# Optimization experiments

Measured on AMD Instinct MI355X. Metric: run time of the kernel, lower is better.

The kernel has to match this reference:

```python
import jax, jax.numpy as jnp
import numpy as np
import math


def setup_inputs() -> dict:
    key = jax.random.key(0)
    kq, kk, kv = jax.random.split(key, 3)
    B, H, S, D = 8, 12, 4096, 64
    q = jax.random.normal(kq, (B, H, S, D), dtype=jnp.float32)
    k = jax.random.normal(kk, (B, H, S, D), dtype=jnp.float32)
    v = jax.random.normal(kv, (B, H, S, D), dtype=jnp.float32)
    return {"q": q, "k": k, "v": v}


def reference(q, k, v):
    B, H, S, D = q.shape
    topk = int(2 * math.sqrt(S))  # 128 for S=4096
    # importance = mean + std (torch.std is unbiased -> ddof=1)
    importance = q.mean(axis=-1) + jnp.std(q, axis=-1, ddof=1)  # [B,H,S]
    _, idx = jax.lax.top_k(importance, topk)  # [B,H,topk]
    idx_e = idx[..., None]  # [B,H,topk,1]
    q_s = jnp.take_along_axis(q, idx_e, axis=2)  # [B,H,topk,D]
    k_s = jnp.take_along_axis(k, idx_e, axis=2)
    v_s = jnp.take_along_axis(v, idx_e, axis=2)
    scores = jnp.einsum('bhtd,bhsd->bhts', q_s, k_s) / math.sqrt(D)
    attn = jax.nn.softmax(scores, axis=-1)
    out_s = jnp.einsum('bhts,bhsd->bhtd', attn, v_s)  # [B,H,topk,D]
    # scatter back into a full tensor (torch uses empty_like; we use zeros
    # for the unselected positions so the output is deterministic)
    bI = jnp.arange(B)[:, None, None]
    hI = jnp.arange(H)[None, :, None]
    out = jnp.zeros_like(v).at[bI, hI, idx].set(out_s)  # [B,H,S,D]
    Himg = int(math.sqrt(S))
    return out.reshape(B, -1, Himg, Himg)  # [B, H*D, Himg, Himg]
```

## Files before the change

### kernel.cpp

```cpp
#include <hip/hip_runtime.h>
#include <hip/hip_fp16.h>
#include <math.h>

#define BH_N 96
#define S_N 4096
#define D_N 64
#define TOPK 128

typedef unsigned long long ull;

__device__ __forceinline__ ull orderKey(double d) {
  ull u = (ull)__double_as_longlong(d);
  if (u & 0x8000000000000000ULL) u = ~u;
  else u |= 0x8000000000000000ULL;
  return u;
}

__global__ __launch_bounds__(256)
void imp_zero_kernel(const float* __restrict__ q, float* __restrict__ out,
                     ull* __restrict__ keys) {
  const int tid = threadIdx.x;
  const size_t off = (size_t)blockIdx.x * 1024 + (size_t)tid * 4;
  const float4 v = *reinterpret_cast<const float4*>(q + off);
  float4 z; z.x = z.y = z.z = z.w = 0.f;
  *reinterpret_cast<float4*>(out + off) = z;

  double s  = (double)v.x + (double)v.y + (double)v.z + (double)v.w;
  double ss = (double)v.x * v.x + (double)v.y * v.y +
              (double)v.z * v.z + (double)v.w * v.w;
#pragma unroll
  for (int m = 1; m < 16; m <<= 1) {
    s  += __shfl_xor(s, m, 64);
    ss += __shfl_xor(ss, m, 64);
  }
  if ((tid & 15) == 0) {
    double mean = s * (1.0 / 64.0);
    double var = (ss - s * s * (1.0 / 64.0)) * (1.0 / 63.0);
    if (var < 0.0) var = 0.0;
    keys[(size_t)blockIdx.x * 16 + (tid >> 4)] = orderKey(mean + sqrt(var));
  }
}

__global__ __launch_bounds__(1024)
void sel_kernel(const ull* __restrict__ keys, int* __restrict__ idx_out) {
  __shared__ int red[2][16];
  __shared__ int s_idx[TOPK];
  __shared__ int s_tidx[1024];
  __shared__ int s_cnt, s_tcnt;

  const int tid = threadIdx.x;
  const int lane = tid & 63;
  const int wv = tid >> 6;
  const int bh = blockIdx.x;
  const ull* kb = keys + (size_t)bh * S_N;

  ull key[4];
#pragma unroll
  for (int i = 0; i < 4; ++i) key[i] = kb[i * 1024 + tid];

  if (tid == 0) { s_cnt = 0; s_tcnt = 0; }

  ull lo = 0ULL, hi = ~0ULL;
  int p = 0;
  while (lo < hi) {
    ull d = hi - lo;
    ull mid = lo + (d >> 1) + (d & 1ULL);
    int c = 0;
#pragma unroll
    for (int i = 0; i < 4; ++i) c += __popcll(__ballot(key[i] >= mid));
    if (lane == 0) red[p][wv] = c;
    __syncthreads();
    int total = 0;
#pragma unroll
    for (int w = 0; w < 16; ++w) total += red[p][w];
    if (total >= TOPK) lo = mid; else hi = mid - 1;
    p ^= 1;
  }
  const ull T = lo;

#pragma unroll
  for (int i = 0; i < 4; ++i) {
    if (key[i] > T) {
      int slot = atomicAdd(&s_cnt, 1);
      s_idx[slot] = i * 1024 + tid;
    } else if (key[i] == T) {
      int sl = atomicAdd(&s_tcnt, 1);
      if (sl < 1024) s_tidx[sl] = i * 1024 + tid;
    }
  }
  __syncthreads();
  const int nsel = s_cnt;
  const int need = TOPK - nsel;
  if (wv == 0 && need > 0) {
    int t = s_tcnt < 1024 ? s_tcnt : 1024;
    for (int sel = 0; sel < need; ++sel) {
      int mymin = 0x7fffffff;
      for (int j = lane; j < t; j += 64) mymin = min(mymin, s_tidx[j]);
#pragma unroll
      for (int m = 1; m < 64; m <<= 1) mymin = min(mymin, __shfl_xor(mymin, m, 64));
      if (lane == 0) s_idx[nsel + sel] = mymin;
      for (int j = lane; j < t; j += 64)
        if (s_tidx[j] == mymin) s_tidx[j] = 0x7fffffff;
    }
  }
  __syncthreads();
  if (tid < TOPK) idx_out[bh * TOPK + tid] = s_idx[tid];
}

__global__ __launch_bounds__(256)
void attn_kernel(const float* __restrict__ q, const float* __restrict__ k,
                 const float* __restrict__ v, const int* __restrict__ idx_all,
                 float* __restrict__ out) {
  __shared__ __align__(16) float sQ[32 * 65];
  __shared__ __align__(16) float sB[64 * 65];
  __shared__ __align__(16) __half sP[32 * 132];
  __shared__ int s_idx[TOPK];

  const int tid = threadIdx.x;
  const int bh = blockIdx.x >> 2;
  const int sub = blockIdx.x & 3;
  if (tid < TOPK) s_idx[tid] = idx_all[bh * TOPK + tid];

  const size_t base = (size_t)bh * S_N * D_N;
  const int rgrp = tid >> 4;
  const int c4 = (tid & 15) * 4;
  const int rr = tid >> 4;
  const int cc = tid & 15;

  __syncthreads();

#pragma unroll
  for (int it = 0; it < 2; ++it) {
    int r = it * 16 + rgrp;
    int srow = s_idx[sub * 32 + r];
    float4 val = *reinterpret_cast<const float4*>(q + base + (size_t)srow * D_N + c4);
    sQ[r * 65 + c4 + 0] = val.x; sQ[r * 65 + c4 + 1] = val.y;
    sQ[r * 65 + c4 + 2] = val.z; sQ[r * 65 + c4 + 3] = val.w;
  }

  float acc[2][8];
#pragma unroll
  for (int j = 0; j < 2; ++j)
#pragma unroll
    for (int m = 0; m < 8; ++m) acc[j][m] = 0.f;

  for (int h = 0; h < 2; ++h) {
    __syncthreads();
#pragma unroll
    for (int it = 0; it < 4; ++it) {
      int r = it * 16 + rgrp;
      int srow = s_idx[h * 64 + r];
      float4 val = *reinterpret_cast<const float4*>(k + base + (size_t)srow * D_N + c4);
      sB[r * 65 + c4 + 0] = val.x; sB[r * 65 + c4 + 1] = val.y;
      sB[r * 65 + c4 + 2] = val.z; sB[r * 65 + c4 + 3] = val.w;
    }
    __syncthreads();
    for (int kk = 0; kk < 64; kk += 2) {
#pragma unroll
      for (int u = 0; u < 2; ++u) {
        float qv0 = sQ[(2 * rr + 0) * 65 + kk + u];
        float qv1 = sQ[(2 * rr + 1) * 65 + kk + u];
        float kv[4];
#pragma unroll
        for (int m = 0; m < 4; ++m) kv[m] = sB[(cc * 4 + m) * 65 + kk + u];
#pragma unroll
        for (int m = 0; m < 4; ++m) {
          acc[0][h * 4 + m] += qv0 * kv[m];
          acc[1][h * 4 + m] += qv1 * kv[m];
        }
      }
    }
  }

  float rmax[2], rsum[2];
#pragma unroll
  for (int j = 0; j < 2; ++j) {
    float mx = acc[j][0];
#pragma unroll
    for (int m = 1; m < 8; ++m) mx = fmaxf(mx, acc[j][m]);
    rmax[j] = mx;
  }
#pragma unroll
  for (int mm = 1; mm < 16; mm <<= 1)
#pragma unroll
    for (int j = 0; j < 2; ++j) rmax[j] = fmaxf(rmax[j], __shfl_xor(rmax[j], mm, 64));
#pragma unroll
  for (int j = 0; j < 2; ++j) {
    float sum = 0.f;
#pragma unroll
    for (int m = 0; m < 8; ++m) {
      float pe = __expf(0.125f * (acc[j][m] - rmax[j]));
      acc[j][m] = pe;
      sum += pe;
    }
    rsum[j] = sum;
  }
#pragma unroll
  for (int mm = 1; mm < 16; mm <<= 1)
#pragma unroll
    for (int j = 0; j < 2; ++j) rsum[j] += __shfl_xor(rsum[j], mm, 64);
#pragma unroll
  for (int j = 0; j < 2; ++j) {
    float rinv = 1.f / rsum[j];
#pragma unroll
    for (int h2 = 0; h2 < 2; ++h2)
#pragma unroll
      for (int m = 0; m < 4; ++m) {
        int col = h2 * 64 + cc * 4 + m;
        sP[(2 * rr + j) * 132 + col] = __float2half_rn(acc[j][h2 * 4 + m] * rinv);
      }
  }

  float acc2[2][4];
#pragma unroll
  for (int j = 0; j < 2; ++j)
#pragma unroll
    for (int m = 0; m < 4; ++m) acc2[j][m] = 0.f;

  for (int h = 0; h < 2; ++h) {
    __syncthreads();
#pragma unroll
    for (int it = 0; it < 4; ++it) {
      int r = it * 16 + rgrp;
      int srow = s_idx[h * 64 + r];
      float4 val = *reinterpret_cast<const float4*>(v + base + (size_t)srow * D_N + c4);
      sB[r * 65 + c4 + 0] = val.x; sB[r * 65 + c4 + 1] = val.y;
      sB[r * 65 + c4 + 2] = val.z; sB[r * 65 + c4 + 3] = val.w;
    }
    __syncthreads();
    for (int s2 = 0; s2 < 64; ++s2) {
      int scol = h * 64 + s2;
      float pj0 = __half2float(sP[(2 * rr + 0) * 132 + scol]);
      float pj1 = __half2float(sP[(2 * rr + 1) * 132 + scol]);
      float vm[4];
#pragma unroll
      for (int m = 0; m < 4; ++m) vm[m] = sB[s2 * 65 + cc * 4 + m];
#pragma unroll
      for (int m = 0; m < 4; ++m) {
        acc2[0][m] += pj0 * vm[m];
        acc2[1][m] += pj1 * vm[m];
      }
    }
  }

#pragma unroll
  for (int j = 0; j < 2; ++j) {
    int srow = s_idx[sub * 32 + 2 * rr + j];
    float4 val;
    val.x = acc2[j][0]; val.y = acc2[j][1]; val.z = acc2[j][2]; val.w = acc2[j][3];
    *reinterpret_cast<float4*>(out + base + (size_t)srow * D_N + cc * 4) = val;
  }
}

extern "C" void kernel_launch(void* const* d_in, const int* in_sizes, int n_in,
                              void* d_out, int out_size, void* d_ws, size_t ws_size,
                              hipStream_t stream) {
  const float* q = (const float*)d_in[0];
  const float* k = (const float*)d_in[1];
  const float* v = (const float*)d_in[2];
  float* out = (float*)d_out;
  ull* keys = (ull*)d_ws;
  int* idx = (int*)((char*)d_ws + (size_t)BH_N * S_N * 8);

  imp_zero_kernel<<<24576, 256, 0, stream>>>(q, out, keys);
  sel_kernel<<<BH_N, 1024, 0, stream>>>(keys, idx);
  attn_kernel<<<BH_N * 4, 256, 0, stream>>>(q, k, v, idx, out);
}
```

Measured before the change: 308.2 us.

## Fuse importance, top-k selection and attention into one cooperative kernel

Merges the three kernels into one cooperative launch of 384 blocks. Each block computes importance keys and zeroes the output for its slice, then waits at a grid-wide sync, then redoes the top-k threshold search for its (b,h) inside a 256-thread block and runs the attention directly. Tie handling moves from a serial min-extraction loop to ballot-based prefix ranking, so the index buffer in global memory is no longer needed. In exchange the selection work is repeated four times per head and the code depends on cooperative-launch support, with a two-kernel fallback if that launch fails.

```diff
diff --git a/kernel.cpp b/kernel.cpp
--- a/kernel.cpp
+++ b/kernel.cpp
@@ -1,19 +1,299 @@
 #include <hip/hip_runtime.h>
 #include <hip/hip_fp16.h>
+#include <hip/hip_cooperative_groups.h>
 #include <math.h>
 
 #define BH_N 96
 #define S_N 4096
 #define D_N 64
 #define TOPK 128
+#define NBLK 384
+#define UNITS_TOTAL 24576
 
 typedef unsigned long long ull;
+namespace cg = cooperative_groups;
 
 __device__ __forceinline__ ull orderKey(double d) {
   ull u = (ull)__double_as_longlong(d);
   if (u & 0x8000000000000000ULL) u = ~u;
   else u |= 0x8000000000000000ULL;
   return u;
+}
+
+struct SharedMem {
+  int red[2][4];
+  int redG[4], redT[4], redS[4];
+  int s_idx[TOPK];
+  __align__(16) float sB[64 * 65];
+  __align__(16) unsigned char uQP[32 * 132 * 2];
+};
+
+__device__ __forceinline__ void sel_attn_body(
+    const float* __restrict__ q, const float* __restrict__ k,
+    const float* __restrict__ v, const ull* __restrict__ keys,
+    float* __restrict__ out, SharedMem& sm, int bh, int sub) {
+  const int tid = threadIdx.x;
+  const int lane = tid & 63;
+  const int wv = tid >> 6;
+
+  ull key[16];
+  {
+    const ull* kb = keys + (size_t)bh * S_N;
+#pragma unroll
+    for (int j = 0; j < 16; ++j) key[j] = kb[tid * 16 + j];
+  }
+
+  ull lo = 0ULL, hi = ~0ULL;
+  int p = 0;
+  while (lo < hi) {
+    ull d = hi - lo;
+    ull mid = lo + (d >> 1) + (d & 1ULL);
+    int c = 0;
+#pragma unroll
+    for (int j = 0; j < 16; ++j) c += __popcll(__ballot(key[j] >= mid));
+    if (lane == 0) sm.red[p][wv] = c;
+    __syncthreads();
+    int total = sm.red[p][0] + sm.red[p][1] + sm.red[p][2] + sm.red[p][3];
+    if (total >= TOPK) lo = mid; else hi = mid - 1;
+    p ^= 1;
+  }
+  const ull T = lo;
+
+  {
+    int cgt = 0, ctie = 0;
+#pragma unroll
+    for (int j = 0; j < 16; ++j) {
+      cgt  += __popcll(__ballot(key[j] > T));
+      ctie += __popcll(__ballot(key[j] == T));
+    }
+    if (lane == 0) { sm.redG[wv] = cgt; sm.redT[wv] = ctie; }
+  }
+  __syncthreads();
+  const int need = TOPK - (sm.redG[0] + sm.redG[1] + sm.redG[2] + sm.redG[3]);
+  int wTieBase = 0;
+#pragma unroll
+  for (int w = 0; w < 4; ++w) if (w < wv) wTieBase += sm.redT[w];
+
+  const ull below = (1ULL << lane) - 1ULL;
+  unsigned selBits = 0;
+  {
+    int lanesBelowTies = 0;
+#pragma unroll
+    for (int j = 0; j < 16; ++j)
+      lanesBelowTies += __popcll(__ballot(key[j] == T) & below);
+    int sameLane = 0;
+#pragma unroll
+    for (int j = 0; j < 16; ++j) {
+      const bool isTie = (key[j] == T);
+      const bool sel = (key[j] > T) ||
+                       (isTie && (wTieBase + lanesBelowTies + sameLane) < need);
+      if (sel) selBits |= (1u << j);
+      sameLane += isTie ? 1 : 0;
+    }
+  }
+
+  {
+    int csel = 0, lanesBelowSel = 0;
+#pragma unroll
+    for (int j = 0; j < 16; ++j) {
+      const ull ms = __ballot((selBits >> j) & 1u);
+      csel += __popcll(ms);
+      lanesBelowSel += __popcll(ms & below);
+    }
+    if (lane == 0) sm.redS[wv] = csel;
+    __syncthreads();
+    int pos = lanesBelowSel;
+#pragma unroll
+    for (int w = 0; w < 4; ++w) if (w < wv) pos += sm.redS[w];
+#pragma unroll
+    for (int j = 0; j < 16; ++j) {
+      if ((selBits >> j) & 1u) { sm.s_idx[pos] = tid * 16 + j; ++pos; }
+    }
+  }
+  __syncthreads();
+
+  float* sQ = reinterpret_cast<float*>(sm.uQP);
+  __half* sP = reinterpret_cast<__half*>(sm.uQP);
+  float* sB = sm.sB;
+
+  const size_t base = (size_t)bh * S_N * D_N;
+  const int rgrp = tid >> 4;
+  const int c4 = (tid & 15) * 4;
+  const int rr = tid >> 4;
+  const int cc = tid & 15;
+
+#pragma unroll
+  for (int it = 0; it < 2; ++it) {
+    int r = it * 16 + rgrp;
+    int srow = sm.s_idx[sub * 32 + r];
+    float4 val = *reinterpret_cast<const float4*>(q + base + (size_t)srow * D_N + c4);
+    sQ[r * 65 + c4 + 0] = val.x; sQ[r * 65 + c4 + 1] = val.y;
+    sQ[r * 65 + c4 + 2] = val.z; sQ[r * 65 + c4 + 3] = val.w;
+  }
+
+  float acc[2][8];
+#pragma unroll
+  for (int j = 0; j < 2; ++j)
+#pragma unroll
+    for (int m = 0; m < 8; ++m) acc[j][m] = 0.f;
+
+  for (int h = 0; h < 2; ++h) {
+    __syncthreads();
+#pragma unroll
+    for (int it = 0; it < 4; ++it) {
+      int r = it * 16 + rgrp;
+      int srow = sm.s_idx[h * 64 + r];
+      float4 val = *reinterpret_cast<const float4*>(k + base + (size_t)srow * D_N + c4);
+      sB[r * 65 + c4 + 0] = val.x; sB[r * 65 + c4 + 1] = val.y;
+      sB[r * 65 + c4 + 2] = val.z; sB[r * 65 + c4 + 3] = val.w;
+    }
+    __syncthreads();
+    for (int kk = 0; kk < 64; kk += 2) {
+#pragma unroll
+      for (int u = 0; u < 2; ++u) {
+        float qv0 = sQ[(2 * rr + 0) * 65 + kk + u];
+        float qv1 = sQ[(2 * rr + 1) * 65 + kk + u];
+        float kv[4];
+#pragma unroll
+        for (int m = 0; m < 4; ++m) kv[m] = sB[(cc * 4 + m) * 65 + kk + u];
+#pragma unroll
+        for (int m = 0; m < 4; ++m) {
+          acc[0][h * 4 + m] += qv0 * kv[m];
+          acc[1][h * 4 + m] += qv1 * kv[m];
+        }
+      }
+    }
+  }
+
+  float rmax[2], rsum[2];
+#pragma unroll
+  for (int j = 0; j < 2; ++j) {
+    float mx = acc[j][0];
+#pragma unroll
+    for (int m = 1; m < 8; ++m) mx = fmaxf(mx, acc[j][m]);
+    rmax[j] = mx;
+  }
+#pragma unroll
+  for (int mm = 1; mm < 16; mm <<= 1)
+#pragma unroll
+    for (int j = 0; j < 2; ++j) rmax[j] = fmaxf(rmax[j], __shfl_xor(rmax[j], mm, 64));
+#pragma unroll
+  for (int j = 0; j < 2; ++j) {
+    float sum = 0.f;
+#pragma unroll
+    for (int m = 0; m < 8; ++m) {
+      float pe = __expf(0.125f * (acc[j][m] - rmax[j]));
+      acc[j][m] = pe;
+      sum += pe;
+    }
+    rsum[j] = sum;
+  }
+#pragma unroll
+  for (int mm = 1; mm < 16; mm <<= 1)
+#pragma unroll
+    for (int j = 0; j < 2; ++j) rsum[j] += __shfl_xor(rsum[j], mm, 64);
+
+  __syncthreads();
+
+#pragma unroll
+  for (int j = 0; j < 2; ++j) {
+    float rinv = 1.f / rsum[j];
+#pragma unroll
+    for (int h2 = 0; h2 < 2; ++h2)
+#pragma unroll
+      for (int m = 0; m < 4; ++m) {
+        int col = h2 * 64 + cc * 4 + m;
+        sP[(2 * rr + j) * 132 + col] = __float2half_rn(acc[j][h2 * 4 + m] * rinv);
+      }
+  }
+
+  float acc2[2][4];
+#pragma unroll
+  for (int j = 0; j < 2; ++j)
+#pragma unroll
+    for (int m = 0; m < 4; ++m) acc2[j][m] = 0.f;
+
+  for (int h = 0; h < 2; ++h) {
+    __syncthreads();
+#pragma unroll
+    for (int it = 0; it < 4; ++it) {
+      int r = it * 16 + rgrp;
+      int srow = sm.s_idx[h * 64 + r];
+      float4 val = *reinterpret_cast<const float4*>(v + base + (size_t)srow * D_N + c4);
+      sB[r * 65 + c4 + 0] = val.x; sB[r * 65 + c4 + 1] = val.y;
+      sB[r * 65 + c4 + 2] = val.z; sB[r * 65 + c4 + 3] = val.w;
+    }
+    __syncthreads();
+    for (int s2 = 0; s2 < 64; ++s2) {
+      int scol = h * 64 + s2;
+      float pj0 = __half2float(sP[(2 * rr + 0) * 132 + scol]);
+      float pj1 = __half2float(sP[(2 * rr + 1) * 132 + scol]);
+      float vm[4];
+#pragma unroll
+      for (int m = 0; m < 4; ++m) vm[m] = sB[s2 * 65 + cc * 4 + m];
+#pragma unroll
+      for (int m = 0; m < 4; ++m) {
+        acc2[0][m] += pj0 * vm[m];
+        acc2[1][m] += pj1 * vm[m];
+      }
+    }
+  }
+
+#pragma unroll
+  for (int j = 0; j < 2; ++j) {
+    int srow = sm.s_idx[sub * 32 + 2 * rr + j];
+    float4 val;
+    val.x = acc2[j][0]; val.y = acc2[j][1]; val.z = acc2[j][2]; val.w = acc2[j][3];
+    *reinterpret_cast<float4*>(out + base + (size_t)srow * D_N + cc * 4) = val;
+  }
+}
+
+__global__ __launch_bounds__(256, 2)
+void fused_coop(const float* __restrict__ q, const float* __restrict__ k,
+                const float* __restrict__ v, float* __restrict__ out,
+                ull* __restrict__ keys) {
+  __shared__ SharedMem sm;
+  {
+    const int bid = blockIdx.x;
+    const int tid = threadIdx.x;
+    float4 z; z.x = z.y = z.z = z.w = 0.f;
+#pragma unroll 1
+    for (int u0 = 0; u0 < UNITS_TOTAL / NBLK; u0 += 8) {
+      size_t offs[8];
+      float4 val[8];
+#pragma unroll
+      for (int i = 0; i < 8; ++i) {
+        const size_t unit = (size_t)bid * (UNITS_TOTAL / NBLK) + (u0 + i);
+        offs[i] = unit * 1024 + (size_t)tid * 4;
+        val[i] = *reinterpret_cast<const float4*>(q + offs[i]);
+      }
+#pragma unroll
+      for (int i = 0; i < 8; ++i)
+        *reinterpret_cast<float4*>(out + offs[i]) = z;
+#pragma unroll
+      for (int i = 0; i < 8; ++i) {
+        double s  = (double)val[i].x + (double)val[i].y + (double)val[i].z + (double)val[i].w;
+        double ss = (double)val[i].x * val[i].x + (double)val[i].y * val[i].y +
+                    (double)val[i].z * val[i].z + (double)val[i].w * val[i].w;
+#pragma unroll
+        for (int m = 1; m < 16; m <<= 1) {
+          s  += __shfl_xor(s, m, 64);
+          ss += __shfl_xor(ss, m, 64);
+        }
+        if ((tid & 15) == 0) {
+          double mean = s * (1.0 / 64.0);
+          double var = (ss - s * s * (1.0 / 64.0)) * (1.0 / 63.0);
+          if (var < 0.0) var = 0.0;
+          const size_t unit = (size_t)bid * (UNITS_TOTAL / NBLK) + (u0 + i);
+          keys[unit * 16 + (tid >> 4)] = orderKey(mean + sqrt(var));
+        }
+      }
+    }
+  }
+
+  cg::this_grid().sync();
+
+  sel_attn_body(q, k, v, keys, out, sm, blockIdx.x >> 2, blockIdx.x & 3);
 }
 
 __global__ __launch_bounds__(256)
@@ -41,215 +321,12 @@
   }
 }
 
-__global__ __launch_bounds__(1024)
-void sel_kernel(const ull* __restrict__ keys, int* __restrict__ idx_out) {
-  __shared__ int red[2][16];
-  __shared__ int s_idx[TOPK];
-  __shared__ int s_tidx[1024];
-  __shared__ int s_cnt, s_tcnt;
-
-  const int tid = threadIdx.x;
-  const int lane = tid & 63;
-  const int wv = tid >> 6;
-  const int bh = blockIdx.x;
-  const ull* kb = keys + (size_t)bh * S_N;
-
-  ull key[4];
-#pragma unroll
-  for (int i = 0; i < 4; ++i) key[i] = kb[i * 1024 + tid];
-
-  if (tid == 0) { s_cnt = 0; s_tcnt = 0; }
-
-  ull lo = 0ULL, hi = ~0ULL;
-  int p = 0;
-  while (lo < hi) {
-    ull d = hi - lo;
-    ull mid = lo + (d >> 1) + (d & 1ULL);
-    int c = 0;
-#pragma unroll
-    for (int i = 0; i < 4; ++i) c += __popcll(__ballot(key[i] >= mid));
-    if (lane == 0) red[p][wv] = c;
-    __syncthreads();
-    int total = 0;
-#pragma unroll
-    for (int w = 0; w < 16; ++w) total += red[p][w];
-    if (total >= TOPK) lo = mid; else hi = mid - 1;
-    p ^= 1;
-  }
-  const ull T = lo;
-
-#pragma unroll
-  for (int i = 0; i < 4; ++i) {
-    if (key[i] > T) {
-      int slot = atomicAdd(&s_cnt, 1);
-      s_idx[slot] = i * 1024 + tid;
-    } else if (key[i] == T) {
-      int sl = atomicAdd(&s_tcnt, 1);
-      if (sl < 1024) s_tidx[sl] = i * 1024 + tid;
-    }
-  }
-  __syncthreads();
-  const int nsel = s_cnt;
-  const int need = TOPK - nsel;
-  if (wv == 0 && need > 0) {
-    int t = s_tcnt < 1024 ? s_tcnt : 1024;
-    for (int sel = 0; sel < need; ++sel) {
-      int mymin = 0x7fffffff;
-      for (int j = lane; j < t; j += 64) mymin = min(mymin, s_tidx[j]);
-#pragma unroll
-      for (int m = 1; m < 64; m <<= 1) mymin = min(mymin, __shfl_xor(mymin, m, 64));
-      if (lane == 0) s_idx[nsel + sel] = mymin;
-      for (int j = lane; j < t; j += 64)
-        if (s_tidx[j] == mymin) s_tidx[j] = 0x7fffffff;
-    }
-  }
-  __syncthreads();
-  if (tid < TOPK) idx_out[bh * TOPK + tid] = s_idx[tid];
-}
-
-__global__ __launch_bounds__(256)
-void attn_kernel(const float* __restrict__ q, const float* __restrict__ k,
-                 const float* __restrict__ v, const int* __restrict__ idx_all,
-                 float* __restrict__ out) {
-  __shared__ __align__(16) float sQ[32 * 65];
-  __shared__ __align__(16) float sB[64 * 65];
-  __shared__ __align__(16) __half sP[32 * 132];
-  __shared__ int s_idx[TOPK];
-
-  const int tid = threadIdx.x;
-  const int bh = blockIdx.x >> 2;
-  const int sub = blockIdx.x & 3;
-  if (tid < TOPK) s_idx[tid] = idx_all[bh * TOPK + tid];
-
-  const size_t base = (size_t)bh * S_N * D_N;
-  const int rgrp = tid >> 4;
-  const int c4 = (tid & 15) * 4;
-  const int rr = tid >> 4;
-  const int cc = tid & 15;
-
-  __syncthreads();
-
-#pragma unroll
-  for (int it = 0; it < 2; ++it) {
-    int r = it * 16 + rgrp;
-    int srow = s_idx[sub * 32 + r];
-    float4 val = *reinterpret_cast<const float4*>(q + base + (size_t)srow * D_N + c4);
-    sQ[r * 65 + c4 + 0] = val.x; sQ[r * 65 + c4 + 1] = val.y;
-    sQ[r * 65 + c4 + 2] = val.z; sQ[r * 65 + c4 + 3] = val.w;
-  }
-
-  float acc[2][8];
-#pragma unroll
-  for (int j = 0; j < 2; ++j)
-#pragma unroll
-    for (int m = 0; m < 8; ++m) acc[j][m] = 0.f;
-
-  for (int h = 0; h < 2; ++h) {
-    __syncthreads();
-#pragma unroll
-    for (int it = 0; it < 4; ++it) {
-      int r = it * 16 + rgrp;
-      int srow = s_idx[h * 64 + r];
-      float4 val = *reinterpret_cast<const float4*>(k + base + (size_t)srow * D_N + c4);
-      sB[r * 65 + c4 + 0] = val.x; sB[r * 65 + c4 + 1] = val.y;
-      sB[r * 65 + c4 + 2] = val.z; sB[r * 65 + c4 + 3] = val.w;
-    }
-    __syncthreads();
-    for (int kk = 0; kk < 64; kk += 2) {
-#pragma unroll
-      for (int u = 0; u < 2; ++u) {
-        float qv0 = sQ[(2 * rr + 0) * 65 + kk + u];
-        float qv1 = sQ[(2 * rr + 1) * 65 + kk + u];
-        float kv[4];
-#pragma unroll
-        for (int m = 0; m < 4; ++m) kv[m] = sB[(cc * 4 + m) * 65 + kk + u];
-#pragma unroll
-        for (int m = 0; m < 4; ++m) {
-          acc[0][h * 4 + m] += qv0 * kv[m];
-          acc[1][h * 4 + m] += qv1 * kv[m];
-        }
-      }
-    }
-  }
-
-  float rmax[2], rsum[2];
-#pragma unroll
-  for (int j = 0; j < 2; ++j) {
-    float mx = acc[j][0];
-#pragma unroll
-    for (int m = 1; m < 8; ++m) mx = fmaxf(mx, acc[j][m]);
-    rmax[j] = mx;
-  }
-#pragma unroll
-  for (int mm = 1; mm < 16; mm <<= 1)
-#pragma unroll
-    for (int j = 0; j < 2; ++j) rmax[j] = fmaxf(rmax[j], __shfl_xor(rmax[j], mm, 64));
-#pragma unroll
-  for (int j = 0; j < 2; ++j) {
-    float sum = 0.f;
-#pragma unroll
-    for (int m = 0; m < 8; ++m) {
-      float pe = __expf(0.125f * (acc[j][m] - rmax[j]));
-      acc[j][m] = pe;
-      sum += pe;
-    }
-    rsum[j] = sum;
-  }
-#pragma unroll
-  for (int mm = 1; mm < 16; mm <<= 1)
-#pragma unroll
-    for (int j = 0; j < 2; ++j) rsum[j] += __shfl_xor(rsum[j], mm, 64);
-#pragma unroll
-  for (int j = 0; j < 2; ++j) {
-    float rinv = 1.f / rsum[j];
-#pragma unroll
-    for (int h2 = 0; h2 < 2; ++h2)
-#pragma unroll
-      for (int m = 0; m < 4; ++m) {
-        int col = h2 * 64 + cc * 4 + m;
-        sP[(2 * rr + j) * 132 + col] = __float2half_rn(acc[j][h2 * 4 + m] * rinv);
-      }
-  }
-
-  float acc2[2][4];
-#pragma unroll
-  for (int j = 0; j < 2; ++j)
-#pragma unroll
-    for (int m = 0; m < 4; ++m) acc2[j][m] = 0.f;
-
-  for (int h = 0; h < 2; ++h) {
-    __syncthreads();
-#pragma unroll
-    for (int it = 0; it < 4; ++it) {
-      int r = it * 16 + rgrp;
-      int srow = s_idx[h * 64 + r];
-      float4 val = *reinterpret_cast<const float4*>(v + base + (size_t)srow * D_N + c4);
-      sB[r * 65 + c4 + 0] = val.x; sB[r * 65 + c4 + 1] = val.y;
-      sB[r * 65 + c4 + 2] = val.z; sB[r * 65 + c4 + 3] = val.w;
-    }
-    __syncthreads();
-    for (int s2 = 0; s2 < 64; ++s2) {
-      int scol = h * 64 + s2;
-      float pj0 = __half2float(sP[(2 * rr + 0) * 132 + scol]);
-      float pj1 = __half2float(sP[(2 * rr + 1) * 132 + scol]);
-      float vm[4];
-#pragma unroll
-      for (int m = 0; m < 4; ++m) vm[m] = sB[s2 * 65 + cc * 4 + m];
-#pragma unroll
-      for (int m = 0; m < 4; ++m) {
-        acc2[0][m] += pj0 * vm[m];
-        acc2[1][m] += pj1 * vm[m];
-      }
-    }
-  }
-
-#pragma unroll
-  for (int j = 0; j < 2; ++j) {
-    int srow = s_idx[sub * 32 + 2 * rr + j];
-    float4 val;
-    val.x = acc2[j][0]; val.y = acc2[j][1]; val.z = acc2[j][2]; val.w = acc2[j][3];
-    *reinterpret_cast<float4*>(out + base + (size_t)srow * D_N + cc * 4) = val;
-  }
+__global__ __launch_bounds__(256, 2)
+void sel_attn_kernel(const float* __restrict__ q, const float* __restrict__ k,
+                     const float* __restrict__ v, const ull* __restrict__ keys,
+                     float* __restrict__ out) {
+  __shared__ SharedMem sm;
+  sel_attn_body(q, k, v, keys, out, sm, blockIdx.x >> 2, blockIdx.x & 3);
 }
 
 extern "C" void kernel_launch(void* const* d_in, const int* in_sizes, int n_in,
@@ -260,9 +337,17 @@
   const float* v = (const float*)d_in[2];
   float* out = (float*)d_out;
   ull* keys = (ull*)d_ws;
-  int* idx = (int*)((char*)d_ws + (size_t)BH_N * S_N * 8);
-
-  imp_zero_kernel<<<24576, 256, 0, stream>>>(q, out, keys);
-  sel_kernel<<<BH_N, 1024, 0, stream>>>(keys, idx);
-  attn_kernel<<<BH_N * 4, 256, 0, stream>>>(q, k, v, idx, out);
-}
+
+  static int coop_ok = -1;
+  if (coop_ok != 0) {
+    void* args[] = {(void*)&q, (void*)&k, (void*)&v, (void*)&out, (void*)&keys};
+    hipError_t e = hipLaunchCooperativeKernel((void*)fused_coop, dim3(NBLK),
+                                              dim3(256), args, 0, stream);
+    if (e == hipSuccess) { coop_ok = 1; return; }
+    coop_ok = 0;
+    (void)hipGetLastError();
+  }
+
+  imp_zero_kernel<<<UNITS_TOTAL, 256, 0, stream>>>(q, out, keys);
+  sel_attn_kernel<<<NBLK, 256, 0, stream>>>(q, k, v, keys, out);
+}
```

Result: faster. 293.4 us (-4.8%).
